# Performance work log

Measured on AMD Instinct MI355X. Metric: run time of the kernel, lower is better.

Reference implementation:

```python
import jax, jax.numpy as jnp
import numpy as np

B, T, C = 2, 2048, 2048
N_HEADS, HEAD_DIM, N_KV_HEADS = 16, 128, 4
N_REP = N_HEADS // N_KV_HEADS
WINDOW = 512
EPS = 1e-6
THETA = 10000.0


def setup_inputs() -> dict:
    key = jax.random.key(0)
    ks = jax.random.split(key, 6)
    x = jax.random.normal(ks[0], (B, T, C), dtype=jnp.float32)
    norm_w = jnp.ones((C,), dtype=jnp.float32)
    wq = jax.random.normal(ks[1], (C, N_HEADS * HEAD_DIM), dtype=jnp.float32) * 0.02
    wk = jax.random.normal(ks[2], (C, N_KV_HEADS * HEAD_DIM), dtype=jnp.float32) * 0.02
    wv = jax.random.normal(ks[3], (C, N_KV_HEADS * HEAD_DIM), dtype=jnp.float32) * 0.02
    wo = jax.random.normal(ks[4], (N_HEADS * HEAD_DIM, C), dtype=jnp.float32) * 0.02
    # precompute_rope: freqs over half head_dim, outer with positions
    inv = 1.0 / (THETA ** (np.arange(0, HEAD_DIM, 2, dtype=np.float32) / HEAD_DIM))
    t = np.arange(T, dtype=np.float32)
    freqs = np.outer(t, inv)  # (T, HEAD_DIM/2)
    rope_cos = jnp.asarray(np.cos(freqs), dtype=jnp.float32)
    rope_sin = jnp.asarray(np.sin(freqs), dtype=jnp.float32)
    return {"x": x, "norm_w": norm_w, "wq": wq, "wk": wk, "wv": wv, "wo": wo,
            "rope_cos": rope_cos, "rope_sin": rope_sin}


def _rmsnorm(x, w):
    xf = x.astype(jnp.float32)
    norm = jax.lax.rsqrt(jnp.mean(xf * xf, axis=-1, keepdims=True) + EPS)
    return (xf * norm).astype(x.dtype) * w


def _rotate(x, cos, sin):
    # x: (B,H,T,D); cos/sin: (1,1,T,D/2). Half-split RoPE as in apply_rope.
    d = x.shape[-1] // 2
    x1, x2 = x[..., :d], x[..., d:]
    return jnp.concatenate([x1 * cos - x2 * sin, x2 * cos + x1 * sin], axis=-1)


def reference(x, norm_w, wq, wk, wv, wo, rope_cos, rope_sin):
    normed = _rmsnorm(x, norm_w)
    q = (normed @ wq).reshape(B, T, N_HEADS, HEAD_DIM).transpose(0, 2, 1, 3)
    k = (normed @ wk).reshape(B, T, N_KV_HEADS, HEAD_DIM).transpose(0, 2, 1, 3)
    v = (normed @ wv).reshape(B, T, N_KV_HEADS, HEAD_DIM).transpose(0, 2, 1, 3)
    cos = rope_cos[None, None, :T, :]
    sin = rope_sin[None, None, :T, :]
    q = _rotate(q, cos, sin)
    k = _rotate(k, cos, sin)
    # GQA: repeat each kv head contiguously (matches expand+reshape)
    k = jnp.repeat(k, N_REP, axis=1)
    v = jnp.repeat(v, N_REP, axis=1)
    scale = 1.0 / jnp.sqrt(jnp.float32(HEAD_DIM))
    scores = jnp.einsum('bhtd,bhsd->bhts', q, k) * scale  # (B,H,T,T)
    # causal + sliding window mask (S == T, offset == 0)
    row = jnp.arange(T)[:, None]
    col = jnp.arange(T)[None, :]
    mask = (col <= row) & (row - col < WINDOW)  # (T,T) bool
    scores = jnp.where(mask[None, None, :, :], scores, -jnp.inf)
    attn = jax.nn.softmax(scores, axis=-1)
    out = jnp.einsum('bhts,bhsd->bhtd', attn, v)
    out = out.transpose(0, 2, 1, 3).reshape(B, T, N_HEADS * HEAD_DIM)
    return x + out @ wo
```

## Files before the change

### kernel.cpp

```cpp
#include <hip/hip_runtime.h>
#include <hip/hip_bf16.h>

typedef __attribute__((ext_vector_type(8))) __bf16 bf16x8;
typedef __attribute__((ext_vector_type(4))) __bf16 bf16x4;
typedef __attribute__((ext_vector_type(4))) float f32x4;

#define BDIM 2
#define TSEQ 2048
#define CDIM 2048
#define NH 16
#define NKV 4
#define HD 128
#define WIN 512

__global__ __launch_bounds__(256) void k_rmsnorm(const float* __restrict__ x,
                                                 const float* __restrict__ w,
                                                 __bf16* __restrict__ xn) {
  __shared__ float red[4];
  const int row = blockIdx.x;
  const int tid = threadIdx.x;
  const float* xr = x + (size_t)row * CDIM;
  f32x4 v0 = *reinterpret_cast<const f32x4*>(&xr[tid * 8]);
  f32x4 v1 = *reinterpret_cast<const f32x4*>(&xr[tid * 8 + 4]);
  float s = v0[0] * v0[0] + v0[1] * v0[1] + v0[2] * v0[2] + v0[3] * v0[3] +
            v1[0] * v1[0] + v1[1] * v1[1] + v1[2] * v1[2] + v1[3] * v1[3];
#pragma unroll
  for (int off = 32; off > 0; off >>= 1) s += __shfl_down(s, off, 64);
  if ((tid & 63) == 0) red[tid >> 6] = s;
  __syncthreads();
  float tot = red[0] + red[1] + red[2] + red[3];
  float nrm = rsqrtf(tot * (1.0f / CDIM) + 1e-6f);
  const float* wp = w + tid * 8;
  bf16x8 o;
  o[0] = (__bf16)(v0[0] * nrm * wp[0]);
  o[1] = (__bf16)(v0[1] * nrm * wp[1]);
  o[2] = (__bf16)(v0[2] * nrm * wp[2]);
  o[3] = (__bf16)(v0[3] * nrm * wp[3]);
  o[4] = (__bf16)(v1[0] * nrm * wp[4]);
  o[5] = (__bf16)(v1[1] * nrm * wp[5]);
  o[6] = (__bf16)(v1[2] * nrm * wp[6]);
  o[7] = (__bf16)(v1[3] * nrm * wp[7]);
  *reinterpret_cast<bf16x8*>(&xn[(size_t)row * CDIM + tid * 8]) = o;
}

__global__ __launch_bounds__(256) void k_wtrans(const float* __restrict__ W,
                                                __bf16* __restrict__ Wt, int N) {
  __shared__ float lt[64][65];
  const int tid = threadIdx.x;
  const int n0 = blockIdx.x * 64, k0 = blockIdx.y * 64;
  const int tr = tid >> 4, tc = tid & 15;
#pragma unroll
  for (int i = 0; i < 4; ++i) {
    int kr = tr + i * 16;
    f32x4 vv = *reinterpret_cast<const f32x4*>(&W[(size_t)(k0 + kr) * N + n0 + tc * 4]);
    lt[kr][tc * 4 + 0] = vv[0];
    lt[kr][tc * 4 + 1] = vv[1];
    lt[kr][tc * 4 + 2] = vv[2];
    lt[kr][tc * 4 + 3] = vv[3];
  }
  __syncthreads();
#pragma unroll
  for (int i = 0; i < 4; ++i) {
    int nr = tr + i * 16;
    int kc = tc * 4;
    bf16x4 o;
    o[0] = (__bf16)lt[kc + 0][nr];
    o[1] = (__bf16)lt[kc + 1][nr];
    o[2] = (__bf16)lt[kc + 2][nr];
    o[3] = (__bf16)lt[kc + 3][nr];
    *reinterpret_cast<bf16x4*>(&Wt[(size_t)(n0 + nr) * 2048 + k0 + kc]) = o;
  }
}

__global__ __launch_bounds__(256) void k_rope(__bf16* __restrict__ Q,
                                              __bf16* __restrict__ K,
                                              const float* __restrict__ rc,
                                              const float* __restrict__ rs) {
  int g = blockIdx.x * 4 + (threadIdx.x >> 6);
  int lane = threadIdx.x & 63;
  int b = g / (TSEQ * (NH + NKV));
  int rem = g % (TSEQ * (NH + NKV));
  int t = rem / (NH + NKV);
  int hh = rem % (NH + NKV);
  __bf16* base;
  if (hh < NH)
    base = Q + (((size_t)(b * NH + hh)) * TSEQ + t) * HD;
  else
    base = K + (((size_t)(b * NKV + (hh - NH))) * TSEQ + t) * HD;
  float x1 = (float)base[lane];
  float x2 = (float)base[lane + 64];
  float c = rc[t * 64 + lane];
  float s = rs[t * 64 + lane];
  base[lane] = (__bf16)(x1 * c - x2 * s);
  base[lane + 64] = (__bf16)(x2 * c + x1 * s);
}

__global__ __launch_bounds__(256) void k_gemm_qkv(
    const __bf16* __restrict__ xn, const __bf16* __restrict__ wqT,
    const __bf16* __restrict__ wkT, const __bf16* __restrict__ wvT,
    __bf16* __restrict__ Q, __bf16* __restrict__ K, __bf16* __restrict__ V) {
  __shared__ __align__(16) __bf16 lA[128][40];
  __shared__ __align__(16) __bf16 lB[128][40];
  const int tid = threadIdx.x;
  const int lane = tid & 63;
  const int wid = tid >> 6;
  const int wrow = (wid >> 1) * 64, wcol = (wid & 1) * 64;
  const int l16 = lane & 15, lhi = lane >> 4;
  const int m0 = blockIdx.y * 128;
  const int n0 = blockIdx.x * 128;
  const __bf16* wt;
  int nrel;
  if (n0 < 2048) { wt = wqT; nrel = n0; }
  else if (n0 < 2560) { wt = wkT; nrel = n0 - 2048; }
  else { wt = wvT; nrel = n0 - 2560; }

  f32x4 acc[4][4] = {};

  for (int k0 = 0; k0 < CDIM; k0 += 32) {
#pragma unroll
    for (int i = 0; i < 2; ++i) {
      int slot = tid + i * 256;
      int r = slot >> 2, c = (slot & 3) * 8;
      *reinterpret_cast<bf16x8*>(&lA[r][c]) =
          *reinterpret_cast<const bf16x8*>(&xn[(size_t)(m0 + r) * CDIM + k0 + c]);
      *reinterpret_cast<bf16x8*>(&lB[r][c]) =
          *reinterpret_cast<const bf16x8*>(&wt[(size_t)(nrel + r) * CDIM + k0 + c]);
    }
    __syncthreads();
    bf16x8 a[4], b[4];
#pragma unroll
    for (int mi = 0; mi < 4; ++mi)
      a[mi] = *reinterpret_cast<const bf16x8*>(&lA[wrow + mi * 16 + l16][lhi * 8]);
#pragma unroll
    for (int ni = 0; ni < 4; ++ni)
      b[ni] = *reinterpret_cast<const bf16x8*>(&lB[wcol + ni * 16 + l16][lhi * 8]);
#pragma unroll
    for (int mi = 0; mi < 4; ++mi)
#pragma unroll
      for (int ni = 0; ni < 4; ++ni)
        acc[mi][ni] = __builtin_amdgcn_mfma_f32_16x16x32_bf16(a[mi], b[ni], acc[mi][ni], 0, 0, 0);
    __syncthreads();
  }

#pragma unroll
  for (int mi = 0; mi < 4; ++mi) {
#pragma unroll
    for (int ni = 0; ni < 4; ++ni) {
#pragma unroll
      for (int r = 0; r < 4; ++r) {
        int row = m0 + wrow + mi * 16 + lhi * 4 + r;
        int col = n0 + wcol + ni * 16 + l16;
        int bb = row >> 11, t = row & 2047;
        __bf16 hv = (__bf16)acc[mi][ni][r];
        if (col < 2048) {
          int h = col >> 7, d = col & 127;
          Q[(((size_t)(bb * NH + h)) * TSEQ + t) * HD + d] = hv;
        } else if (col < 2560) {
          int h = (col - 2048) >> 7, d = col & 127;
          K[(((size_t)(bb * NKV + h)) * TSEQ + t) * HD + d] = hv;
        } else {
          int h = (col - 2560) >> 7, d = col & 127;
          V[(((size_t)(bb * NKV + h)) * TSEQ + t) * HD + d] = hv;
        }
      }
    }
  }
}

__global__ __launch_bounds__(256) void k_attn(const __bf16* __restrict__ Q,
                                              const __bf16* __restrict__ K,
                                              const __bf16* __restrict__ V,
                                              __bf16* __restrict__ Aout) {
  __shared__ __align__(16) __bf16 lK[32][136];
  __shared__ __align__(16) __bf16 lVt[128][40];
  __shared__ __align__(16) __bf16 lP[4][16][40];

  const int tid = threadIdx.x, lane = tid & 63, wid = tid >> 6;
  const int l16 = lane & 15, lhi = lane >> 4;
  const int bh = blockIdx.y;
  const int b = bh >> 4, h = bh & 15;
  const int kvh = h >> 2;
  const int q0 = blockIdx.x * 64;
  const int qw = q0 + wid * 16;

  const __bf16* Qb = Q + (size_t)bh * TSEQ * HD;
  const __bf16* Kb = K + (size_t)(b * NKV + kvh) * TSEQ * HD;
  const __bf16* Vb = V + (size_t)(b * NKV + kvh) * TSEQ * HD;

  bf16x8 aq[4];
#pragma unroll
  for (int dblk = 0; dblk < 4; ++dblk)
    aq[dblk] = *reinterpret_cast<const bf16x8*>(&Qb[(size_t)(qw + l16) * HD + dblk * 32 + lhi * 8]);

  float mrow[4], lrow[4];
#pragma unroll
  for (int r = 0; r < 4; ++r) { mrow[r] = -INFINITY; lrow[r] = 0.0f; }
  f32x4 accO[8] = {};

  int s_lo = q0 - (WIN - 1);
  if (s_lo < 0) s_lo = 0;
  s_lo &= ~31;
  const float scale = 0.08838834764831845f;

  for (int s0 = s_lo; s0 < q0 + 64; s0 += 32) {
#pragma unroll
    for (int i = 0; i < 2; ++i) {
      int slot = tid + i * 256;
      int kr = slot >> 4, kc = (slot & 15) * 8;
      *reinterpret_cast<bf16x8*>(&lK[kr][kc]) =
          *reinterpret_cast<const bf16x8*>(&Kb[(size_t)(s0 + kr) * HD + kc]);
      int vr = slot & 31, vc = (slot >> 5) * 8;
      bf16x8 vv = *reinterpret_cast<const bf16x8*>(&Vb[(size_t)(s0 + vr) * HD + vc]);
#pragma unroll
      for (int j = 0; j < 8; ++j) lVt[vc + j][vr] = vv[j];
    }
    __syncthreads();

    f32x4 accS[2] = {};
#pragma unroll
    for (int sb = 0; sb < 2; ++sb) {
#pragma unroll
      for (int dblk = 0; dblk < 4; ++dblk) {
        bf16x8 bk = *reinterpret_cast<const bf16x8*>(&lK[sb * 16 + l16][dblk * 32 + lhi * 8]);
        accS[sb] = __builtin_amdgcn_mfma_f32_16x16x32_bf16(aq[dblk], bk, accS[sb], 0, 0, 0);
      }
    }

    float p0s[4], p1s[4];
#pragma unroll
    for (int r = 0; r < 4; ++r) {
      int qrow = qw + lhi * 4 + r;
      int sc0 = s0 + l16, sc1 = s0 + 16 + l16;
      float v0 = accS[0][r] * scale;
      float v1 = accS[1][r] * scale;
      bool ok0 = (sc0 <= qrow) && (qrow - sc0 < WIN);
      bool ok1 = (sc1 <= qrow) && (qrow - sc1 < WIN);
      v0 = ok0 ? v0 : -INFINITY;
      v1 = ok1 ? v1 : -INFINITY;
      float tmax = fmaxf(v0, v1);
#pragma unroll
      for (int off = 1; off < 16; off <<= 1) tmax = fmaxf(tmax, __shfl_xor(tmax, off, 64));
      float mnew = fmaxf(mrow[r], tmax);
      float msafe = (mnew == -INFINITY) ? 0.0f : mnew;
      float corr = (mrow[r] == mnew) ? 1.0f : __expf(mrow[r] - mnew);
      float p0 = __expf(v0 - msafe);
      float p1 = __expf(v1 - msafe);
      float psum = p0 + p1;
#pragma unroll
      for (int off = 1; off < 16; off <<= 1) psum += __shfl_xor(psum, off, 64);
      lrow[r] = lrow[r] * corr + psum;
      mrow[r] = mnew;
#pragma unroll
      for (int ni = 0; ni < 8; ++ni) accO[ni][r] *= corr;
      p0s[r] = p0;
      p1s[r] = p1;
    }

#pragma unroll
    for (int r = 0; r < 4; ++r) {
      lP[wid][lhi * 4 + r][l16] = (__bf16)p0s[r];
      lP[wid][lhi * 4 + r][16 + l16] = (__bf16)p1s[r];
    }
    bf16x8 ap = *reinterpret_cast<const bf16x8*>(&lP[wid][l16][lhi * 8]);
#pragma unroll
    for (int ni = 0; ni < 8; ++ni) {
      bf16x8 bv = *reinterpret_cast<const bf16x8*>(&lVt[ni * 16 + l16][lhi * 8]);
      accO[ni] = __builtin_amdgcn_mfma_f32_16x16x32_bf16(ap, bv, accO[ni], 0, 0, 0);
    }
    __syncthreads();
  }

  float invl[4];
#pragma unroll
  for (int r = 0; r < 4; ++r) invl[r] = 1.0f / lrow[r];
#pragma unroll
  for (int ni = 0; ni < 8; ++ni) {
#pragma unroll
    for (int r = 0; r < 4; ++r) {
      int row = qw + lhi * 4 + r;
      int d = ni * 16 + l16;
      Aout[((size_t)(b * TSEQ + row)) * CDIM + h * HD + d] = (__bf16)(accO[ni][r] * invl[r]);
    }
  }
}

__global__ __launch_bounds__(256) void k_gemm_out(const __bf16* __restrict__ A,
                                                  const __bf16* __restrict__ woT,
                                                  const float* __restrict__ x,
                                                  float* __restrict__ out) {
  __shared__ __align__(16) __bf16 lA[128][40];
  __shared__ __align__(16) __bf16 lB[128][40];
  const int tid = threadIdx.x;
  const int lane = tid & 63;
  const int wid = tid >> 6;
  const int wrow = (wid >> 1) * 64, wcol = (wid & 1) * 64;
  const int l16 = lane & 15, lhi = lane >> 4;
  const int m0 = blockIdx.y * 128;
  const int n0 = blockIdx.x * 128;

  f32x4 acc[4][4] = {};

  for (int k0 = 0; k0 < CDIM; k0 += 32) {
#pragma unroll
    for (int i = 0; i < 2; ++i) {
      int slot = tid + i * 256;
      int r = slot >> 2, c = (slot & 3) * 8;
      *reinterpret_cast<bf16x8*>(&lA[r][c]) =
          *reinterpret_cast<const bf16x8*>(&A[(size_t)(m0 + r) * CDIM + k0 + c]);
      *reinterpret_cast<bf16x8*>(&lB[r][c]) =
          *reinterpret_cast<const bf16x8*>(&woT[(size_t)(n0 + r) * CDIM + k0 + c]);
    }
    __syncthreads();
    bf16x8 a[4], b[4];
#pragma unroll
    for (int mi = 0; mi < 4; ++mi)
      a[mi] = *reinterpret_cast<const bf16x8*>(&lA[wrow + mi * 16 + l16][lhi * 8]);
#pragma unroll
    for (int ni = 0; ni < 4; ++ni)
      b[ni] = *reinterpret_cast<const bf16x8*>(&lB[wcol + ni * 16 + l16][lhi * 8]);
#pragma unroll
    for (int mi = 0; mi < 4; ++mi)
#pragma unroll
      for (int ni = 0; ni < 4; ++ni)
        acc[mi][ni] = __builtin_amdgcn_mfma_f32_16x16x32_bf16(a[mi], b[ni], acc[mi][ni], 0, 0, 0);
    __syncthreads();
  }

#pragma unroll
  for (int mi = 0; mi < 4; ++mi) {
#pragma unroll
    for (int ni = 0; ni < 4; ++ni) {
#pragma unroll
      for (int r = 0; r < 4; ++r) {
        int row = m0 + wrow + mi * 16 + lhi * 4 + r;
        int col = n0 + wcol + ni * 16 + l16;
        size_t idx = (size_t)row * CDIM + col;
        out[idx] = x[idx] + acc[mi][ni][r];
      }
    }
  }
}

extern "C" void kernel_launch(void* const* d_in, const int* in_sizes, int n_in,
                              void* d_out, int out_size, void* d_ws, size_t ws_size,
                              hipStream_t stream) {
  const float* x = (const float*)d_in[0];
  const float* norm_w = (const float*)d_in[1];
  const float* wq = (const float*)d_in[2];
  const float* wk = (const float*)d_in[3];
  const float* wv = (const float*)d_in[4];
  const float* wo = (const float*)d_in[5];
  const float* rc = (const float*)d_in[6];
  const float* rs = (const float*)d_in[7];
  float* out = (float*)d_out;

  char* ws = (char*)d_ws;
  __bf16* xn  = (__bf16*)(ws);
  __bf16* wqT = (__bf16*)(ws + 16777216);
  __bf16* wkT = (__bf16*)(ws + 25165824);
  __bf16* wvT = (__bf16*)(ws + 27262976);
  __bf16* woT = (__bf16*)(ws + 29360128);
  __bf16* Qb  = (__bf16*)(ws + 37748736);
  __bf16* Kb  = (__bf16*)(ws + 54525952);
  __bf16* Vb  = (__bf16*)(ws + 58720256);
  if (ws_size < 62914560) return;

  k_wtrans<<<dim3(32, 32), 256, 0, stream>>>(wq, wqT, 2048);
  k_wtrans<<<dim3(8, 32), 256, 0, stream>>>(wk, wkT, 512);
  k_wtrans<<<dim3(8, 32), 256, 0, stream>>>(wv, wvT, 512);
  k_wtrans<<<dim3(32, 32), 256, 0, stream>>>(wo, woT, 2048);
  k_rmsnorm<<<4096, 256, 0, stream>>>(x, norm_w, xn);
  k_gemm_qkv<<<dim3(24, 32), 256, 0, stream>>>(xn, wqT, wkT, wvT, Qb, Kb, Vb);
  k_rope<<<(BDIM * TSEQ * (NH + NKV)) / 4, 256, 0, stream>>>(Qb, Kb, rc, rs);
  k_attn<<<dim3(TSEQ / 64, BDIM * NH), 256, 0, stream>>>(Qb, Kb, Vb, xn);
  k_gemm_out<<<dim3(16, 32), 256, 0, stream>>>(xn, woT, x, out);
}
```

Before: 344.2 us.

## Use direct global-to-LDS loads in GEMMs, store V transposed, widen attention KV tile

Both GEMM kernels now load their tiles with global_load_lds straight into an unpadded LDS layout, so the data no longer passes through registers. The QKV GEMM writes V already transposed (d-major), which lets attention fill its V^T tile with vector loads instead of scalar transposing LDS stores. Attention now processes 64 keys per iteration instead of 32, halving the number of barriers and loop iterations. The trade-offs are possible LDS bank conflicts from dropping the row padding, uncoalesced scattered stores when writing V^T, and more wasted masked work at the window edges.

```diff
diff --git a/kernel.cpp b/kernel.cpp
--- a/kernel.cpp
+++ b/kernel.cpp
@@ -12,6 +12,12 @@
 #define NKV 4
 #define HD 128
 #define WIN 512
+
+__device__ __forceinline__ void gl_lds16(const __bf16* g, __bf16* l) {
+  __builtin_amdgcn_global_load_lds(
+      (const __attribute__((address_space(1))) void*)g,
+      (__attribute__((address_space(3))) void*)l, 16, 0, 0);
+}
 
 __global__ __launch_bounds__(256) void k_rmsnorm(const float* __restrict__ x,
                                                  const float* __restrict__ w,
@@ -98,14 +104,16 @@
 __global__ __launch_bounds__(256) void k_gemm_qkv(
     const __bf16* __restrict__ xn, const __bf16* __restrict__ wqT,
     const __bf16* __restrict__ wkT, const __bf16* __restrict__ wvT,
-    __bf16* __restrict__ Q, __bf16* __restrict__ K, __bf16* __restrict__ V) {
-  __shared__ __align__(16) __bf16 lA[128][40];
-  __shared__ __align__(16) __bf16 lB[128][40];
+    __bf16* __restrict__ Q, __bf16* __restrict__ K, __bf16* __restrict__ VT) {
+  __shared__ __align__(16) __bf16 lA[128 * 32];
+  __shared__ __align__(16) __bf16 lB[128 * 32];
   const int tid = threadIdx.x;
   const int lane = tid & 63;
-  const int wid = tid >> 6;
-  const int wrow = (wid >> 1) * 64, wcol = (wid & 1) * 64;
+  const int w = tid >> 6;
+  const int wrow = (w >> 1) * 64, wcol = (w & 1) * 64;
   const int l16 = lane & 15, lhi = lane >> 4;
+  const int grow = lane >> 2;
+  const int gcol = (lane & 3) * 8;
   const int m0 = blockIdx.y * 128;
   const int n0 = blockIdx.x * 128;
   const __bf16* wt;
@@ -119,21 +127,18 @@
   for (int k0 = 0; k0 < CDIM; k0 += 32) {
 #pragma unroll
     for (int i = 0; i < 2; ++i) {
-      int slot = tid + i * 256;
-      int r = slot >> 2, c = (slot & 3) * 8;
-      *reinterpret_cast<bf16x8*>(&lA[r][c]) =
-          *reinterpret_cast<const bf16x8*>(&xn[(size_t)(m0 + r) * CDIM + k0 + c]);
-      *reinterpret_cast<bf16x8*>(&lB[r][c]) =
-          *reinterpret_cast<const bf16x8*>(&wt[(size_t)(nrel + r) * CDIM + k0 + c]);
+      const int r0 = (w * 2 + i) * 16;
+      gl_lds16(&xn[(size_t)(m0 + r0 + grow) * CDIM + k0 + gcol], &lA[r0 * 32]);
+      gl_lds16(&wt[(size_t)(nrel + r0 + grow) * CDIM + k0 + gcol], &lB[r0 * 32]);
     }
     __syncthreads();
     bf16x8 a[4], b[4];
 #pragma unroll
     for (int mi = 0; mi < 4; ++mi)
-      a[mi] = *reinterpret_cast<const bf16x8*>(&lA[wrow + mi * 16 + l16][lhi * 8]);
+      a[mi] = *reinterpret_cast<const bf16x8*>(&lA[(wrow + mi * 16 + l16) * 32 + lhi * 8]);
 #pragma unroll
     for (int ni = 0; ni < 4; ++ni)
-      b[ni] = *reinterpret_cast<const bf16x8*>(&lB[wcol + ni * 16 + l16][lhi * 8]);
+      b[ni] = *reinterpret_cast<const bf16x8*>(&lB[(wcol + ni * 16 + l16) * 32 + lhi * 8]);
 #pragma unroll
     for (int mi = 0; mi < 4; ++mi)
 #pragma unroll
@@ -160,7 +165,7 @@
           K[(((size_t)(bb * NKV + h)) * TSEQ + t) * HD + d] = hv;
         } else {
           int h = (col - 2560) >> 7, d = col & 127;
-          V[(((size_t)(bb * NKV + h)) * TSEQ + t) * HD + d] = hv;
+          VT[(((size_t)(bb * NKV + h)) * HD + d) * TSEQ + t] = hv;
         }
       }
     }
@@ -169,11 +174,11 @@
 
 __global__ __launch_bounds__(256) void k_attn(const __bf16* __restrict__ Q,
                                               const __bf16* __restrict__ K,
-                                              const __bf16* __restrict__ V,
+                                              const __bf16* __restrict__ VT,
                                               __bf16* __restrict__ Aout) {
-  __shared__ __align__(16) __bf16 lK[32][136];
-  __shared__ __align__(16) __bf16 lVt[128][40];
-  __shared__ __align__(16) __bf16 lP[4][16][40];
+  __shared__ __align__(16) __bf16 lK[64][136];
+  __shared__ __align__(16) __bf16 lVt[128][72];
+  __shared__ __align__(16) __bf16 lP[4][16][72];
 
   const int tid = threadIdx.x, lane = tid & 63, wid = tid >> 6;
   const int l16 = lane & 15, lhi = lane >> 4;
@@ -185,7 +190,7 @@
 
   const __bf16* Qb = Q + (size_t)bh * TSEQ * HD;
   const __bf16* Kb = K + (size_t)(b * NKV + kvh) * TSEQ * HD;
-  const __bf16* Vb = V + (size_t)(b * NKV + kvh) * TSEQ * HD;
+  const __bf16* Vt = VT + (size_t)(b * NKV + kvh) * HD * TSEQ;
 
   bf16x8 aq[4];
 #pragma unroll
@@ -199,26 +204,25 @@
 
   int s_lo = q0 - (WIN - 1);
   if (s_lo < 0) s_lo = 0;
-  s_lo &= ~31;
+  s_lo &= ~63;
   const float scale = 0.08838834764831845f;
 
-  for (int s0 = s_lo; s0 < q0 + 64; s0 += 32) {
-#pragma unroll
-    for (int i = 0; i < 2; ++i) {
+  for (int s0 = s_lo; s0 < q0 + 64; s0 += 64) {
+#pragma unroll
+    for (int i = 0; i < 4; ++i) {
       int slot = tid + i * 256;
       int kr = slot >> 4, kc = (slot & 15) * 8;
       *reinterpret_cast<bf16x8*>(&lK[kr][kc]) =
           *reinterpret_cast<const bf16x8*>(&Kb[(size_t)(s0 + kr) * HD + kc]);
-      int vr = slot & 31, vc = (slot >> 5) * 8;
-      bf16x8 vv = *reinterpret_cast<const bf16x8*>(&Vb[(size_t)(s0 + vr) * HD + vc]);
-#pragma unroll
-      for (int j = 0; j < 8; ++j) lVt[vc + j][vr] = vv[j];
-    }
-    __syncthreads();
-
-    f32x4 accS[2] = {};
-#pragma unroll
-    for (int sb = 0; sb < 2; ++sb) {
+      int vd = slot >> 3, vc = (slot & 7) * 8;
+      *reinterpret_cast<bf16x8*>(&lVt[vd][vc]) =
+          *reinterpret_cast<const bf16x8*>(&Vt[(size_t)vd * TSEQ + s0 + vc]);
+    }
+    __syncthreads();
+
+    f32x4 accS[4] = {};
+#pragma unroll
+    for (int sb = 0; sb < 4; ++sb) {
 #pragma unroll
       for (int dblk = 0; dblk < 4; ++dblk) {
         bf16x8 bk = *reinterpret_cast<const bf16x8*>(&lK[sb * 16 + l16][dblk * 32 + lhi * 8]);
@@ -226,46 +230,53 @@
       }
     }
 
-    float p0s[4], p1s[4];
 #pragma unroll
     for (int r = 0; r < 4; ++r) {
       int qrow = qw + lhi * 4 + r;
-      int sc0 = s0 + l16, sc1 = s0 + 16 + l16;
-      float v0 = accS[0][r] * scale;
-      float v1 = accS[1][r] * scale;
-      bool ok0 = (sc0 <= qrow) && (qrow - sc0 < WIN);
-      bool ok1 = (sc1 <= qrow) && (qrow - sc1 < WIN);
-      v0 = ok0 ? v0 : -INFINITY;
-      v1 = ok1 ? v1 : -INFINITY;
-      float tmax = fmaxf(v0, v1);
+      float vv[4];
+      float tmax = -INFINITY;
+#pragma unroll
+      for (int sb = 0; sb < 4; ++sb) {
+        int sc = s0 + sb * 16 + l16;
+        float val = accS[sb][r] * scale;
+        bool ok = (sc <= qrow) && (qrow - sc < WIN);
+        vv[sb] = ok ? val : -INFINITY;
+        tmax = fmaxf(tmax, vv[sb]);
+      }
 #pragma unroll
       for (int off = 1; off < 16; off <<= 1) tmax = fmaxf(tmax, __shfl_xor(tmax, off, 64));
       float mnew = fmaxf(mrow[r], tmax);
       float msafe = (mnew == -INFINITY) ? 0.0f : mnew;
       float corr = (mrow[r] == mnew) ? 1.0f : __expf(mrow[r] - mnew);
-      float p0 = __expf(v0 - msafe);
-      float p1 = __expf(v1 - msafe);
-      float psum = p0 + p1;
+      float psum = 0.0f;
+#pragma unroll
+      for (int sb = 0; sb < 4; ++sb) {
+        float p = __expf(vv[sb] - msafe);
+        vv[sb] = p;
+        psum += p;
+      }
 #pragma unroll
       for (int off = 1; off < 16; off <<= 1) psum += __shfl_xor(psum, off, 64);
       lrow[r] = lrow[r] * corr + psum;
       mrow[r] = mnew;
 #pragma unroll
       for (int ni = 0; ni < 8; ++ni) accO[ni][r] *= corr;
-      p0s[r] = p0;
-      p1s[r] = p1;
-    }
-
-#pragma unroll
-    for (int r = 0; r < 4; ++r) {
-      lP[wid][lhi * 4 + r][l16] = (__bf16)p0s[r];
-      lP[wid][lhi * 4 + r][16 + l16] = (__bf16)p1s[r];
-    }
-    bf16x8 ap = *reinterpret_cast<const bf16x8*>(&lP[wid][l16][lhi * 8]);
+#pragma unroll
+      for (int sb = 0; sb < 4; ++sb)
+        lP[wid][lhi * 4 + r][sb * 16 + l16] = (__bf16)vv[sb];
+    }
+
+    bf16x8 ap[2];
+#pragma unroll
+    for (int ks = 0; ks < 2; ++ks)
+      ap[ks] = *reinterpret_cast<const bf16x8*>(&lP[wid][l16][ks * 32 + lhi * 8]);
 #pragma unroll
     for (int ni = 0; ni < 8; ++ni) {
-      bf16x8 bv = *reinterpret_cast<const bf16x8*>(&lVt[ni * 16 + l16][lhi * 8]);
-      accO[ni] = __builtin_amdgcn_mfma_f32_16x16x32_bf16(ap, bv, accO[ni], 0, 0, 0);
+#pragma unroll
+      for (int ks = 0; ks < 2; ++ks) {
+        bf16x8 bv = *reinterpret_cast<const bf16x8*>(&lVt[ni * 16 + l16][ks * 32 + lhi * 8]);
+        accO[ni] = __builtin_amdgcn_mfma_f32_16x16x32_bf16(ap[ks], bv, accO[ni], 0, 0, 0);
+      }
     }
     __syncthreads();
   }
@@ -288,13 +299,15 @@
                                                   const __bf16* __restrict__ woT,
                                                   const float* __restrict__ x,
                                                   float* __restrict__ out) {
-  __shared__ __align__(16) __bf16 lA[128][40];
-  __shared__ __align__(16) __bf16 lB[128][40];
+  __shared__ __align__(16) __bf16 lA[128 * 32];
+  __shared__ __align__(16) __bf16 lB[128 * 32];
   const int tid = threadIdx.x;
   const int lane = tid & 63;
-  const int wid = tid >> 6;
-  const int wrow = (wid >> 1) * 64, wcol = (wid & 1) * 64;
+  const int w = tid >> 6;
+  const int wrow = (w >> 1) * 64, wcol = (w & 1) * 64;
   const int l16 = lane & 15, lhi = lane >> 4;
+  const int grow = lane >> 2;
+  const int gcol = (lane & 3) * 8;
   const int m0 = blockIdx.y * 128;
   const int n0 = blockIdx.x * 128;
 
@@ -303,21 +316,18 @@
   for (int k0 = 0; k0 < CDIM; k0 += 32) {
 #pragma unroll
     for (int i = 0; i < 2; ++i) {
-      int slot = tid + i * 256;
-      int r = slot >> 2, c = (slot & 3) * 8;
-      *reinterpret_cast<bf16x8*>(&lA[r][c]) =
-          *reinterpret_cast<const bf16x8*>(&A[(size_t)(m0 + r) * CDIM + k0 + c]);
-      *reinterpret_cast<bf16x8*>(&lB[r][c]) =
-          *reinterpret_cast<const bf16x8*>(&woT[(size_t)(n0 + r) * CDIM + k0 + c]);
+      const int r0 = (w * 2 + i) * 16;
+      gl_lds16(&A[(size_t)(m0 + r0 + grow) * CDIM + k0 + gcol], &lA[r0 * 32]);
+      gl_lds16(&woT[(size_t)(n0 + r0 + grow) * CDIM + k0 + gcol], &lB[r0 * 32]);
     }
     __syncthreads();
     bf16x8 a[4], b[4];
 #pragma unroll
     for (int mi = 0; mi < 4; ++mi)
-      a[mi] = *reinterpret_cast<const bf16x8*>(&lA[wrow + mi * 16 + l16][lhi * 8]);
+      a[mi] = *reinterpret_cast<const bf16x8*>(&lA[(wrow + mi * 16 + l16) * 32 + lhi * 8]);
 #pragma unroll
     for (int ni = 0; ni < 4; ++ni)
-      b[ni] = *reinterpret_cast<const bf16x8*>(&lB[wcol + ni * 16 + l16][lhi * 8]);
+      b[ni] = *reinterpret_cast<const bf16x8*>(&lB[(wcol + ni * 16 + l16) * 32 + lhi * 8]);
 #pragma unroll
     for (int mi = 0; mi < 4; ++mi)
 #pragma unroll
@@ -362,7 +372,7 @@
   __bf16* woT = (__bf16*)(ws + 29360128);
   __bf16* Qb  = (__bf16*)(ws + 37748736);
   __bf16* Kb  = (__bf16*)(ws + 54525952);
-  __bf16* Vb  = (__bf16*)(ws + 58720256);
+  __bf16* VTb = (__bf16*)(ws + 58720256);
   if (ws_size < 62914560) return;
 
   k_wtrans<<<dim3(32, 32), 256, 0, stream>>>(wq, wqT, 2048);
@@ -370,8 +380,8 @@
   k_wtrans<<<dim3(8, 32), 256, 0, stream>>>(wv, wvT, 512);
   k_wtrans<<<dim3(32, 32), 256, 0, stream>>>(wo, woT, 2048);
   k_rmsnorm<<<4096, 256, 0, stream>>>(x, norm_w, xn);
-  k_gemm_qkv<<<dim3(24, 32), 256, 0, stream>>>(xn, wqT, wkT, wvT, Qb, Kb, Vb);
+  k_gemm_qkv<<<dim3(24, 32), 256, 0, stream>>>(xn, wqT, wkT, wvT, Qb, Kb, VTb);
   k_rope<<<(BDIM * TSEQ * (NH + NKV)) / 4, 256, 0, stream>>>(Qb, Kb, rc, rs);
-  k_attn<<<dim3(TSEQ / 64, BDIM * NH), 256, 0, stream>>>(Qb, Kb, Vb, xn);
+  k_attn<<<dim3(TSEQ / 64, BDIM * NH), 256, 0, stream>>>(Qb, Kb, VTb, xn);
   k_gemm_out<<<dim3(16, 32), 256, 0, stream>>>(xn, woT, x, out);
 }
```

Result: no change. 346.4 us (+0.6%).
